# Performance work log

Hardware: AMD Instinct MI355X
Metric: run time of the kernel (lower is better)

Reference implementation:

```python
import jax, jax.numpy as jnp
import numpy as np

V = 32000       # word vocab size
K = 24          # max n-grams per word (n=3, word len <= 9 -> 3*len-3 <= 24)
NG = 200000     # n_gram_size (hash table size)
E = 128         # emb_size
B, S = 16, 2048 # batch, seq_len


def setup_inputs() -> dict:
    key = jax.random.key(0)
    k1, k2, k3, k4 = jax.random.split(key, 4)
    word_idx = jax.random.randint(k1, (B, S), 0, V, dtype=jnp.int32)
    # hashed n-gram ids live in [4, NG), matching _hash(word) % (NG-4) + 4
    ngram_ids = jax.random.randint(k2, (V, K), 4, NG, dtype=jnp.int32)
    ngram_counts = jax.random.randint(k3, (V,), 1, K + 1, dtype=jnp.int32)
    # pad unused slots with id 0 (padding_idx -> zero embedding row)
    pos = jnp.arange(K)[None, :]
    ngram_ids = jnp.where(pos < ngram_counts[:, None], ngram_ids, 0)
    # special tokens (<4): direct lookup of their own embedding row, count 1
    sp = jnp.arange(4)
    ngram_ids = ngram_ids.at[sp, :].set(0).at[sp, 0].set(sp)
    ngram_counts = ngram_counts.at[sp].set(1)
    emb_table = jax.random.normal(k4, (NG, E), dtype=jnp.float32)
    return {"word_idx": word_idx, "ngram_ids": ngram_ids,
            "ngram_counts": ngram_counts, "emb_table": emb_table}


def reference(word_idx, ngram_ids, ngram_counts, emb_table):
    # nn.Embedding(padding_idx=0): row 0 is zero
    table = emb_table.at[0].set(0.0)
    g = ngram_ids[word_idx]                 # [B, S, K] gathered n-gram ids
    e = table[g]                            # [B, S, K, E] gathered embeddings
    cnt = ngram_counts[word_idx].astype(e.dtype)[..., None]  # [B, S, 1]
    # padded slots point at the zero row, so a plain sum == masked sum
    return e.sum(axis=2) / cnt              # [B, S, E] mean over n-grams
```

## Files before the change

kernel.cpp:

```cpp
#include <hip/hip_runtime.h>

#define NUM_WORDS 32768
#define KMAX 24

__global__ __launch_bounds__(256) void ngram_emb_kernel(
    const int* __restrict__ word_idx,
    const int* __restrict__ ngram_ids,
    const int* __restrict__ ngram_counts,
    const float* __restrict__ emb_table,
    float* __restrict__ out)
{
    const int gtid = blockIdx.x * blockDim.x + threadIdx.x;
    const int word = gtid >> 6;
    const int lane = threadIdx.x & 63;

    const int w   = __builtin_amdgcn_readfirstlane(word_idx[word]);
    const int cnt = ngram_counts[w];
    const int* ids = ngram_ids + w * KMAX;

    int rr[KMAX];
#pragma unroll
    for (int k = 0; k < KMAX; ++k)
        rr[k] = __builtin_amdgcn_readfirstlane(ids[k]);

    const float2* tbl = (const float2*)emb_table;

    float2 v[KMAX];
#pragma unroll
    for (int j = 0; j < 8; ++j)
        v[j] = tbl[(long)rr[j] * 64 + lane];
    if (cnt > 8) {
#pragma unroll
        for (int j = 8; j < 16; ++j)
            v[j] = tbl[(long)rr[j] * 64 + lane];
    }
    if (cnt > 16) {
#pragma unroll
        for (int j = 16; j < 24; ++j)
            v[j] = tbl[(long)rr[j] * 64 + lane];
    }

    float ax = 0.f, ay = 0.f;
#pragma unroll
    for (int j = 0; j < 8; ++j) {
        const float m = rr[j] ? 1.f : 0.f;
        ax = fmaf(m, v[j].x, ax);
        ay = fmaf(m, v[j].y, ay);
    }
    if (cnt > 8) {
#pragma unroll
        for (int j = 8; j < 16; ++j) {
            const float m = rr[j] ? 1.f : 0.f;
            ax = fmaf(m, v[j].x, ax);
            ay = fmaf(m, v[j].y, ay);
        }
    }
    if (cnt > 16) {
#pragma unroll
        for (int j = 16; j < 24; ++j) {
            const float m = rr[j] ? 1.f : 0.f;
            ax = fmaf(m, v[j].x, ax);
            ay = fmaf(m, v[j].y, ay);
        }
    }

    const float inv = 1.0f / (float)cnt;
    float2 o; o.x = ax * inv; o.y = ay * inv;
    ((float2*)out)[(long)word * 64 + lane] = o;
}

extern "C" void kernel_launch(void* const* d_in, const int* in_sizes, int n_in,
                              void* d_out, int out_size, void* d_ws, size_t ws_size,
                              hipStream_t stream) {
    const int*   word_idx     = (const int*)d_in[0];
    const int*   ngram_ids    = (const int*)d_in[1];
    const int*   ngram_counts = (const int*)d_in[2];
    const float* emb_table    = (const float*)d_in[3];
    float*       out          = (float*)d_out;

    const int threads = 256;
    const int blocks  = (NUM_WORDS * 64) / threads;
    ngram_emb_kernel<<<blocks, threads, 0, stream>>>(
        word_idx, ngram_ids, ngram_counts, emb_table, out);
}
```

Before: 169.3 us.

## Deduplicate repeated words so each unique word's n-gram gather runs once

Adds a workspace table, sized to the vocabulary, that records one owner position per distinct word index, filled by an atomicCAS pass. The main kernel then does the n-gram embedding gather and mean only for owner positions. A final kernel copies the owner's output row into every duplicate position. The aim is to cut the redundant random-row gather traffic for repeated words. The cost is two small extra launches, atomics, and a dependent copy pass that reads back rows written by the previous kernel.

```diff
diff --git a/kernel.cpp b/kernel.cpp
--- a/kernel.cpp
+++ b/kernel.cpp
@@ -1,20 +1,35 @@
 #include <hip/hip_runtime.h>
 
+#define VOCAB 32000
 #define NUM_WORDS 32768
 #define KMAX 24
 
-__global__ __launch_bounds__(256) void ngram_emb_kernel(
+__global__ __launch_bounds__(256) void init_slots(int* __restrict__ slot) {
+    const int i = blockIdx.x * blockDim.x + threadIdx.x;
+    if (i < VOCAB) slot[i] = -1;
+}
+
+__global__ __launch_bounds__(256) void claim_owners(
+    const int* __restrict__ word_idx, int* __restrict__ slot) {
+    const int p = blockIdx.x * blockDim.x + threadIdx.x;
+    if (p < NUM_WORDS) atomicCAS(&slot[word_idx[p]], -1, p);
+}
+
+__global__ __launch_bounds__(256) void ngram_emb_owner_kernel(
     const int* __restrict__ word_idx,
     const int* __restrict__ ngram_ids,
     const int* __restrict__ ngram_counts,
     const float* __restrict__ emb_table,
+    const int* __restrict__ slot,
     float* __restrict__ out)
 {
     const int gtid = blockIdx.x * blockDim.x + threadIdx.x;
-    const int word = gtid >> 6;
+    const int p    = gtid >> 6;
     const int lane = threadIdx.x & 63;
 
-    const int w   = __builtin_amdgcn_readfirstlane(word_idx[word]);
+    const int w = __builtin_amdgcn_readfirstlane(word_idx[p]);
+    if (slot[w] != p) return;
+
     const int cnt = ngram_counts[w];
     const int* ids = ngram_ids + w * KMAX;
 
@@ -66,7 +81,24 @@
 
     const float inv = 1.0f / (float)cnt;
     float2 o; o.x = ax * inv; o.y = ay * inv;
-    ((float2*)out)[(long)word * 64 + lane] = o;
+    ((float2*)out)[(long)p * 64 + lane] = o;
+}
+
+__global__ __launch_bounds__(256) void scatter_dups(
+    const int* __restrict__ word_idx,
+    const int* __restrict__ slot,
+    float* __restrict__ out)
+{
+    const int gtid = blockIdx.x * blockDim.x + threadIdx.x;
+    const int p    = gtid >> 6;
+    const int lane = threadIdx.x & 63;
+
+    const int w     = __builtin_amdgcn_readfirstlane(word_idx[p]);
+    const int owner = slot[w];
+    if (owner == p) return;
+
+    float2* o2 = (float2*)out;
+    o2[(long)p * 64 + lane] = o2[(long)owner * 64 + lane];
 }
 
 extern "C" void kernel_launch(void* const* d_in, const int* in_sizes, int n_in,
@@ -77,9 +109,14 @@
     const int*   ngram_counts = (const int*)d_in[2];
     const float* emb_table    = (const float*)d_in[3];
     float*       out          = (float*)d_out;
+    int*         slot         = (int*)d_ws;
+
+    init_slots<<<(VOCAB + 255) / 256, 256, 0, stream>>>(slot);
+    claim_owners<<<(NUM_WORDS + 255) / 256, 256, 0, stream>>>(word_idx, slot);
 
     const int threads = 256;
     const int blocks  = (NUM_WORDS * 64) / threads;
-    ngram_emb_kernel<<<blocks, threads, 0, stream>>>(
-        word_idx, ngram_ids, ngram_counts, emb_table, out);
+    ngram_emb_owner_kernel<<<blocks, threads, 0, stream>>>(
+        word_idx, ngram_ids, ngram_counts, emb_table, slot, out);
+    scatter_dups<<<blocks, threads, 0, stream>>>(word_idx, slot, out);
 }
```

After: 172.8 us. 1.02x slower.
